# Optimization experiments

Measured on AMD Instinct MI355X. Metric: run time of the kernel, lower is better.

Reference implementation:

```python
import jax, jax.numpy as jnp
import numpy as np

B, C, W, H, D = 1, 2, 192, 192, 192


def setup_inputs() -> dict:
    key = jax.random.key(0)
    k1, k2 = jax.random.split(key)
    x = jax.random.normal(k1, (B, C, W, H, D), dtype=jnp.float32)
    # voxel coordinates, slightly outside the FOV to exercise dct2 boundary
    sizes = jnp.array([W, H, D], dtype=jnp.float32)
    u = jax.random.uniform(k2, (B, W, H, D, 3), dtype=jnp.float32)
    grid = u * (sizes + 3.0) - 2.0  # range [-2, n+1]
    return {"x": x, "grid": grid}


def _reflect_dct2(i, n):
    # dct2 / 'reflect' boundary: symmetric about -0.5 and n-0.5, period 2n
    p = 2 * n
    i = jnp.mod(i, p)  # nonnegative result
    return jnp.where(i >= n, p - 1 - i, i)


def reference(x, grid):
    """grid_pull with linear interpolation, dct2 bound, extrapolate=True.
    x: (B, C, W, H, D); grid: (B, W, H, D, 3) in voxel coords -> (B, C, W, H, D)."""
    Bx, Cx, Wx, Hx, Dx = x.shape
    lo = jnp.floor(grid).astype(jnp.int32)          # (B, W, H, D, 3)
    frac = grid - lo.astype(grid.dtype)             # (B, W, H, D, 3)
    flat = x.reshape(Bx, Cx, Wx * Hx * Dx)
    N = grid.shape[1] * grid.shape[2] * grid.shape[3]
    out = jnp.zeros((Bx, Cx, N), dtype=x.dtype)
    for dx in (0, 1):
        wx = frac[..., 0] if dx else 1.0 - frac[..., 0]
        ix = _reflect_dct2(lo[..., 0] + dx, Wx)
        for dy in (0, 1):
            wy = frac[..., 1] if dy else 1.0 - frac[..., 1]
            iy = _reflect_dct2(lo[..., 1] + dy, Hx)
            for dz in (0, 1):
                wz = frac[..., 2] if dz else 1.0 - frac[..., 2]
                iz = _reflect_dct2(lo[..., 2] + dz, Dx)
                idx = ((ix * Hx + iy) * Dx + iz).reshape(Bx, 1, N)
                vals = jnp.take_along_axis(flat, idx, axis=2)  # (B, C, N)
                w = (wx * wy * wz).reshape(Bx, 1, N)
                out = out + vals * w
    return out.reshape(Bx, Cx, *grid.shape[1:4])
```

## Files before the change

### kernel.cpp

```cpp
#include <hip/hip_runtime.h>
#include <hip/hip_fp16.h>


constexpr int DIM = 192;
constexpr int N = DIM * DIM * DIM;
constexpr int C = 2;

typedef float floatx4 __attribute__((ext_vector_type(4)));

__device__ __forceinline__ int reflect_dct2(int i, int n) {
    const int p = 2 * n;
    i = ((i % p) + p) % p;
    return (i >= n) ? (p - 1 - i) : i;
}

constexpr size_t HALO_BRICKS = (size_t)(DIM / 4) * DIM * DIM;
constexpr size_t HALO_BYTES  = HALO_BRICKS * 64;

constexpr int LDS_STRIDE = 200;

__global__ __launch_bounds__(256) void repack_halo_kernel(
        const float* __restrict__ x,
        uint32_t* __restrict__ xb) {
    __shared__ float lds[16 * LDS_STRIDE];

    const int bxy = blockIdx.x;
    const int y   = bxy % DIM;
    const int bx  = bxy / DIM;
    const int tid = threadIdx.x;

#pragma unroll
    for (int k = 0; k < 3; ++k) {
        const int vidx = tid + k * 256;
        const int r    = vidx / 48;
        const int c4   = vidx - r * 48;
        const int c    = r >> 3;
        const int sx   = (r >> 1) & 3;
        const int ysel = r & 1;
        const int ysrc = min(y + ysel, DIM - 1);
        const size_t src = (size_t)c * N
                         + ((size_t)((bx * 4 + sx) * DIM + ysrc)) * DIM
                         + (size_t)c4 * 4;
        const floatx4 v = __builtin_nontemporal_load((const floatx4*)(x + src));
        *(floatx4*)(&lds[r * LDS_STRIDE + c4 * 4]) = v;
    }
    __syncthreads();

#pragma unroll
    for (int k = 0; k < 3; ++k) {
        const int t  = tid + k * 256;
        const int z  = t >> 2;
        const int q  = t & 3;
        const int zp = min(z + 1, DIM - 1);
        const int r00 = q * 2;
        const int r01 = q * 2 + 1;
        const int r10 = 8 + q * 2;
        const int r11 = 8 + q * 2 + 1;
        uint4 v;
        v.x = __builtin_bit_cast(uint32_t,
              __floats2half2_rn(lds[r00 * LDS_STRIDE + z],  lds[r10 * LDS_STRIDE + z]));
        v.y = __builtin_bit_cast(uint32_t,
              __floats2half2_rn(lds[r00 * LDS_STRIDE + zp], lds[r10 * LDS_STRIDE + zp]));
        v.z = __builtin_bit_cast(uint32_t,
              __floats2half2_rn(lds[r01 * LDS_STRIDE + z],  lds[r11 * LDS_STRIDE + z]));
        v.w = __builtin_bit_cast(uint32_t,
              __floats2half2_rn(lds[r01 * LDS_STRIDE + zp], lds[r11 * LDS_STRIDE + zp]));
        ((uint4*)xb)[(size_t)bxy * (DIM * 4) + t] = v;
    }
}

__global__ __launch_bounds__(256) void grid_pull_halo_kernel(
        const uint32_t* __restrict__ xb,
        const float* __restrict__ grid,
        float* __restrict__ out) {
    const int n = blockIdx.x * blockDim.x + threadIdx.x;
    if (n >= N) return;

    const float gx = __builtin_nontemporal_load(&grid[3 * n + 0]);
    const float gy = __builtin_nontemporal_load(&grid[3 * n + 1]);
    const float gz = __builtin_nontemporal_load(&grid[3 * n + 2]);

    const float fx = floorf(gx), fy = floorf(gy), fz = floorf(gz);
    const int lx = (int)fx, ly = (int)fy, lz = (int)fz;
    const float tx = gx - fx, ty = gy - fy, tz = gz - fz;

    const int ix0 = reflect_dct2(lx,     DIM);
    const int ix1 = reflect_dct2(lx + 1, DIM);
    const int iy0 = reflect_dct2(ly,     DIM);
    const int iy1 = reflect_dct2(ly + 1, DIM);
    const int iz0 = reflect_dct2(lz,     DIM);
    const int iz1 = reflect_dct2(lz + 1, DIM);

    const int ya = min(iy0, iy1), za = min(iz0, iz1);
    const int sy0 = iy0 - ya, sy1 = iy1 - ya;
    const int sz0 = iz0 - za, sz1 = iz1 - za;

    const float wy0 = 1.0f - ty, wy1 = ty;
    const float wz0 = 1.0f - tz, wz1 = tz;

    const float Y0 = (sy0 ? 0.0f : wy0) + (sy1 ? 0.0f : wy1);
    const float Y1 = (sy0 ? wy0 : 0.0f) + (sy1 ? wy1 : 0.0f);
    const float Z0 = (sz0 ? 0.0f : wz0) + (sz1 ? 0.0f : wz1);
    const float Z1 = (sz0 ? wz0 : 0.0f) + (sz1 ? wz1 : 0.0f);

    const size_t d0 = ((size_t)(((ix0 >> 2) * DIM + ya) * DIM + za) << 4) + ((ix0 & 3) << 2);
    const size_t d1 = ((size_t)(((ix1 >> 2) * DIM + ya) * DIM + za) << 4) + ((ix1 & 3) << 2);
    const uint4 v0 = *(const uint4*)(xb + d0);
    const uint4 v1 = *(const uint4*)(xb + d1);

    const float2 a00 = __half22float2(__builtin_bit_cast(__half2, v0.x));
    const float2 a01 = __half22float2(__builtin_bit_cast(__half2, v0.y));
    const float2 a10 = __half22float2(__builtin_bit_cast(__half2, v0.z));
    const float2 a11 = __half22float2(__builtin_bit_cast(__half2, v0.w));
    const float2 b00 = __half22float2(__builtin_bit_cast(__half2, v1.x));
    const float2 b01 = __half22float2(__builtin_bit_cast(__half2, v1.y));
    const float2 b10 = __half22float2(__builtin_bit_cast(__half2, v1.z));
    const float2 b11 = __half22float2(__builtin_bit_cast(__half2, v1.w));

    const float wx0 = 1.0f - tx, wx1 = tx;

    const float acc0 = wx0 * (Y0 * (Z0 * a00.x + Z1 * a01.x) + Y1 * (Z0 * a10.x + Z1 * a11.x))
                     + wx1 * (Y0 * (Z0 * b00.x + Z1 * b01.x) + Y1 * (Z0 * b10.x + Z1 * b11.x));
    const float acc1 = wx0 * (Y0 * (Z0 * a00.y + Z1 * a01.y) + Y1 * (Z0 * a10.y + Z1 * a11.y))
                     + wx1 * (Y0 * (Z0 * b00.y + Z1 * b01.y) + Y1 * (Z0 * b10.y + Z1 * b11.y));

    __builtin_nontemporal_store(acc0, &out[n]);
    __builtin_nontemporal_store(acc1, &out[N + n]);
}

constexpr int NBX = DIM / 4;
constexpr int NBY = DIM / 2;
constexpr int NBZ = DIM / 2;
constexpr int NBRICKS = NBX * NBY * NBZ;
constexpr int XSTRIDE = NBY * NBZ * 16;
constexpr int YSTRIDE = NBZ * 16;
constexpr int ZSTRIDE = 16;

__device__ __forceinline__ int xterm(int ix) { return (ix >> 2) * XSTRIDE + ((ix & 3) << 2); }
__device__ __forceinline__ int yterm(int iy) { return (iy >> 1) * YSTRIDE + ((iy & 1) << 1); }
__device__ __forceinline__ int zterm(int iz) { return (iz >> 1) * ZSTRIDE + (iz & 1); }

__global__ __launch_bounds__(256) void repack_brick_lds_kernel(
        const float* __restrict__ x,
        uint32_t* __restrict__ xb) {
    __shared__ float lds[16 * LDS_STRIDE];

    const int bxy = blockIdx.x;
    const int by  = bxy % NBY;
    const int bx  = bxy / NBY;
    const int tid = threadIdx.x;

#pragma unroll
    for (int k = 0; k < 3; ++k) {
        const int vidx = tid + k * 256;
        const int r    = vidx / 48;
        const int c4   = vidx - r * 48;
        const int c    = r >> 3;
        const int sx   = (r >> 1) & 3;
        const int sy   = r & 1;
        const size_t src = (size_t)c * N
                         + ((size_t)((bx * 4 + sx) * DIM + (by * 2 + sy))) * DIM
                         + (size_t)c4 * 4;
        const floatx4 v = __builtin_nontemporal_load((const floatx4*)(x + src));
        *(floatx4*)(&lds[r * LDS_STRIDE + c4 * 4]) = v;
    }
    __syncthreads();

    for (int slot = tid; slot < NBZ * 4; slot += 256) {
        const int bz = slot >> 2;
        const int q  = slot & 3;
        const int iz = bz * 2;
        const float2 a00 = *(const float2*)&lds[(((0 << 3) | (q << 1) | 0) * LDS_STRIDE) + iz];
        const float2 a01 = *(const float2*)&lds[(((0 << 3) | (q << 1) | 1) * LDS_STRIDE) + iz];
        const float2 a10 = *(const float2*)&lds[(((1 << 3) | (q << 1) | 0) * LDS_STRIDE) + iz];
        const float2 a11 = *(const float2*)&lds[(((1 << 3) | (q << 1) | 1) * LDS_STRIDE) + iz];
        uint4 v;
        v.x = __builtin_bit_cast(uint32_t, __floats2half2_rn(a00.x, a10.x));
        v.y = __builtin_bit_cast(uint32_t, __floats2half2_rn(a00.y, a10.y));
        v.z = __builtin_bit_cast(uint32_t, __floats2half2_rn(a01.x, a11.x));
        v.w = __builtin_bit_cast(uint32_t, __floats2half2_rn(a01.y, a11.y));
        ((uint4*)xb)[(size_t)bxy * (NBZ * 4) + slot] = v;
    }
}

__global__ __launch_bounds__(256) void grid_pull_brick_kernel(
        const uint32_t* __restrict__ xb,
        const float* __restrict__ grid,
        float* __restrict__ out) {
    const int n = blockIdx.x * blockDim.x + threadIdx.x;
    if (n >= N) return;

    const float gx = __builtin_nontemporal_load(&grid[3 * n + 0]);
    const float gy = __builtin_nontemporal_load(&grid[3 * n + 1]);
    const float gz = __builtin_nontemporal_load(&grid[3 * n + 2]);

    const float fx = floorf(gx), fy = floorf(gy), fz = floorf(gz);
    const int lx = (int)fx, ly = (int)fy, lz = (int)fz;
    const float tx = gx - fx, ty = gy - fy, tz = gz - fz;

    const int ix0 = reflect_dct2(lx,     DIM);
    const int ix1 = reflect_dct2(lx + 1, DIM);
    const int iy0 = reflect_dct2(ly,     DIM);
    const int iy1 = reflect_dct2(ly + 1, DIM);
    const int iz0 = reflect_dct2(lz,     DIM);
    const int iz1 = reflect_dct2(lz + 1, DIM);

    const int tx0 = xterm(ix0), tx1 = xterm(ix1);
    const int ty0 = yterm(iy0), ty1 = yterm(iy1);
    const int tz0 = zterm(iz0), tz1 = zterm(iz1);

    const uint32_t u000 = xb[tx0 + ty0 + tz0];
    const uint32_t u001 = xb[tx0 + ty0 + tz1];
    const uint32_t u010 = xb[tx0 + ty1 + tz0];
    const uint32_t u011 = xb[tx0 + ty1 + tz1];
    const uint32_t u100 = xb[tx1 + ty0 + tz0];
    const uint32_t u101 = xb[tx1 + ty0 + tz1];
    const uint32_t u110 = xb[tx1 + ty1 + tz0];
    const uint32_t u111 = xb[tx1 + ty1 + tz1];

    const float wx0 = 1.0f - tx, wx1 = tx;
    const float wy0 = 1.0f - ty, wy1 = ty;
    const float wz0 = 1.0f - tz, wz1 = tz;

    const float w000 = wx0 * wy0 * wz0, w001 = wx0 * wy0 * wz1;
    const float w010 = wx0 * wy1 * wz0, w011 = wx0 * wy1 * wz1;
    const float w100 = wx1 * wy0 * wz0, w101 = wx1 * wy0 * wz1;
    const float w110 = wx1 * wy1 * wz0, w111 = wx1 * wy1 * wz1;

    const float2 f000 = __half22float2(__builtin_bit_cast(__half2, u000));
    const float2 f001 = __half22float2(__builtin_bit_cast(__half2, u001));
    const float2 f010 = __half22float2(__builtin_bit_cast(__half2, u010));
    const float2 f011 = __half22float2(__builtin_bit_cast(__half2, u011));
    const float2 f100 = __half22float2(__builtin_bit_cast(__half2, u100));
    const float2 f101 = __half22float2(__builtin_bit_cast(__half2, u101));
    const float2 f110 = __half22float2(__builtin_bit_cast(__half2, u110));
    const float2 f111 = __half22float2(__builtin_bit_cast(__half2, u111));

    const float acc0 = f000.x * w000 + f001.x * w001 + f010.x * w010 + f011.x * w011
                     + f100.x * w100 + f101.x * w101 + f110.x * w110 + f111.x * w111;
    const float acc1 = f000.y * w000 + f001.y * w001 + f010.y * w010 + f011.y * w011
                     + f100.y * w100 + f101.y * w101 + f110.y * w110 + f111.y * w111;

    __builtin_nontemporal_store(acc0, &out[n]);
    __builtin_nontemporal_store(acc1, &out[N + n]);
}

__global__ __launch_bounds__(256) void grid_pull_planar_kernel(
        const float* __restrict__ x,
        const float* __restrict__ grid,
        float* __restrict__ out) {
    const int n = blockIdx.x * blockDim.x + threadIdx.x;
    if (n >= N) return;

    const float gx = grid[3 * n + 0];
    const float gy = grid[3 * n + 1];
    const float gz = grid[3 * n + 2];

    const float fx = floorf(gx), fy = floorf(gy), fz = floorf(gz);
    const int lx = (int)fx, ly = (int)fy, lz = (int)fz;
    const float tx = gx - fx, ty = gy - fy, tz = gz - fz;

    const int ix0 = reflect_dct2(lx,     DIM);
    const int ix1 = reflect_dct2(lx + 1, DIM);
    const int iy0 = reflect_dct2(ly,     DIM);
    const int iy1 = reflect_dct2(ly + 1, DIM);
    const int iz0 = reflect_dct2(lz,     DIM);
    const int iz1 = reflect_dct2(lz + 1, DIM);

    const float wx0 = 1.0f - tx, wx1 = tx;
    const float wy0 = 1.0f - ty, wy1 = ty;
    const float wz0 = 1.0f - tz, wz1 = tz;

    const int bx0 = ix0 * (DIM * DIM), bx1 = ix1 * (DIM * DIM);
    const int by0 = iy0 * DIM,         by1 = iy1 * DIM;

    const float w000 = wx0 * wy0 * wz0, w001 = wx0 * wy0 * wz1;
    const float w010 = wx0 * wy1 * wz0, w011 = wx0 * wy1 * wz1;
    const float w100 = wx1 * wy0 * wz0, w101 = wx1 * wy0 * wz1;
    const float w110 = wx1 * wy1 * wz0, w111 = wx1 * wy1 * wz1;

#pragma unroll
    for (int c = 0; c < C; ++c) {
        const float* __restrict__ xc = x + (size_t)c * N;
        float acc = xc[bx0 + by0 + iz0] * w000;
        acc += xc[bx0 + by0 + iz1] * w001;
        acc += xc[bx0 + by1 + iz0] * w010;
        acc += xc[bx0 + by1 + iz1] * w011;
        acc += xc[bx1 + by0 + iz0] * w100;
        acc += xc[bx1 + by0 + iz1] * w101;
        acc += xc[bx1 + by1 + iz0] * w110;
        acc += xc[bx1 + by1 + iz1] * w111;
        out[(size_t)c * N + n] = acc;
    }
}

extern "C" void kernel_launch(void* const* d_in, const int* in_sizes, int n_in,
                              void* d_out, int out_size, void* d_ws, size_t ws_size,
                              hipStream_t stream) {
    const float* x    = (const float*)d_in[0];
    const float* grid = (const float*)d_in[1];
    float* out        = (float*)d_out;

    const int threads = 256;
    const int gblocks = (N + threads - 1) / threads;
    const size_t need_brick = (size_t)NBRICKS * 64;

    if (ws_size >= HALO_BYTES) {
        uint32_t* xb = (uint32_t*)d_ws;
        repack_halo_kernel<<<(DIM / 4) * DIM, threads, 0, stream>>>(x, xb);
        grid_pull_halo_kernel<<<gblocks, threads, 0, stream>>>(xb, grid, out);
    } else if (ws_size >= need_brick) {
        uint32_t* xb = (uint32_t*)d_ws;
        repack_brick_lds_kernel<<<NBX * NBY, threads, 0, stream>>>(x, xb);
        grid_pull_brick_kernel<<<gblocks, threads, 0, stream>>>(xb, grid, out);
    } else {
        grid_pull_planar_kernel<<<gblocks, threads, 0, stream>>>(x, grid, out);
    }
}
```

Baseline: 338.2 us.

## Process two y rows per repack block and four voxels per pull thread

The halo repack kernel now handles two consecutive y rows per block, loading three source rows per x/channel into shared memory instead of two per single row. This cuts redundant global reads of the shared y+1 row. The pull kernel gives each thread four consecutive voxels, using three 16-byte vector loads of the grid and vector nontemporal stores of the outputs. This raises memory-level parallelism but increases register use and may lower occupancy.

```diff
diff --git a/kernel.cpp b/kernel.cpp
--- a/kernel.cpp
+++ b/kernel.cpp
@@ -19,43 +19,50 @@
 
 constexpr int LDS_STRIDE = 200;
 
-__global__ __launch_bounds__(256) void repack_halo_kernel(
+__global__ __launch_bounds__(256) void repack_halo2_kernel(
         const float* __restrict__ x,
         uint32_t* __restrict__ xb) {
-    __shared__ float lds[16 * LDS_STRIDE];
-
-    const int bxy = blockIdx.x;
-    const int y   = bxy % DIM;
-    const int bx  = bxy / DIM;
+    __shared__ float lds[24 * LDS_STRIDE];
+
+    const int blk = blockIdx.x;
+    const int yp  = blk % (DIM / 2);
+    const int bx  = blk / (DIM / 2);
+    const int y0  = yp * 2;
     const int tid = threadIdx.x;
 
 #pragma unroll
-    for (int k = 0; k < 3; ++k) {
+    for (int k = 0; k < 5; ++k) {
         const int vidx = tid + k * 256;
-        const int r    = vidx / 48;
-        const int c4   = vidx - r * 48;
-        const int c    = r >> 3;
-        const int sx   = (r >> 1) & 3;
-        const int ysel = r & 1;
-        const int ysrc = min(y + ysel, DIM - 1);
-        const size_t src = (size_t)c * N
-                         + ((size_t)((bx * 4 + sx) * DIM + ysrc)) * DIM
-                         + (size_t)c4 * 4;
-        const floatx4 v = __builtin_nontemporal_load((const floatx4*)(x + src));
-        *(floatx4*)(&lds[r * LDS_STRIDE + c4 * 4]) = v;
+        if (vidx < 24 * 48) {
+            const int r    = vidx / 48;
+            const int c4   = vidx - r * 48;
+            const int c    = r / 12;
+            const int rem  = r - c * 12;
+            const int sx   = rem / 3;
+            const int rsel = rem - sx * 3;
+            const int ysrc = min(y0 + rsel, DIM - 1);
+            const size_t src = (size_t)c * N
+                             + ((size_t)((bx * 4 + sx) * DIM + ysrc)) * DIM
+                             + (size_t)c4 * 4;
+            const floatx4 v = __builtin_nontemporal_load((const floatx4*)(x + src));
+            *(floatx4*)(&lds[r * LDS_STRIDE + c4 * 4]) = v;
+        }
     }
     __syncthreads();
 
 #pragma unroll
-    for (int k = 0; k < 3; ++k) {
+    for (int k = 0; k < 6; ++k) {
         const int t  = tid + k * 256;
-        const int z  = t >> 2;
+        const int a  = t >> 10;
         const int q  = t & 3;
+        const int az = t >> 2;
+        const int aa = az / DIM;
+        const int z  = az - aa * DIM;
         const int zp = min(z + 1, DIM - 1);
-        const int r00 = q * 2;
-        const int r01 = q * 2 + 1;
-        const int r10 = 8 + q * 2;
-        const int r11 = 8 + q * 2 + 1;
+        const int r00 = q * 3 + aa;
+        const int r01 = q * 3 + aa + 1;
+        const int r10 = 12 + q * 3 + aa;
+        const int r11 = 12 + q * 3 + aa + 1;
         uint4 v;
         v.x = __builtin_bit_cast(uint32_t,
               __floats2half2_rn(lds[r00 * LDS_STRIDE + z],  lds[r10 * LDS_STRIDE + z]));
@@ -65,67 +72,83 @@
               __floats2half2_rn(lds[r01 * LDS_STRIDE + z],  lds[r11 * LDS_STRIDE + z]));
         v.w = __builtin_bit_cast(uint32_t,
               __floats2half2_rn(lds[r01 * LDS_STRIDE + zp], lds[r11 * LDS_STRIDE + zp]));
-        ((uint4*)xb)[(size_t)bxy * (DIM * 4) + t] = v;
-    }
-}
-
-__global__ __launch_bounds__(256) void grid_pull_halo_kernel(
+        const size_t brick = ((size_t)(bx * DIM + (y0 + aa)) * DIM + z);
+        ((uint4*)xb)[brick * 4 + q] = v;
+    }
+}
+
+__global__ __launch_bounds__(256) void grid_pull_halo4_kernel(
         const uint32_t* __restrict__ xb,
         const float* __restrict__ grid,
         float* __restrict__ out) {
-    const int n = blockIdx.x * blockDim.x + threadIdx.x;
-    if (n >= N) return;
-
-    const float gx = __builtin_nontemporal_load(&grid[3 * n + 0]);
-    const float gy = __builtin_nontemporal_load(&grid[3 * n + 1]);
-    const float gz = __builtin_nontemporal_load(&grid[3 * n + 2]);
-
-    const float fx = floorf(gx), fy = floorf(gy), fz = floorf(gz);
-    const int lx = (int)fx, ly = (int)fy, lz = (int)fz;
-    const float tx = gx - fx, ty = gy - fy, tz = gz - fz;
-
-    const int ix0 = reflect_dct2(lx,     DIM);
-    const int ix1 = reflect_dct2(lx + 1, DIM);
-    const int iy0 = reflect_dct2(ly,     DIM);
-    const int iy1 = reflect_dct2(ly + 1, DIM);
-    const int iz0 = reflect_dct2(lz,     DIM);
-    const int iz1 = reflect_dct2(lz + 1, DIM);
-
-    const int ya = min(iy0, iy1), za = min(iz0, iz1);
-    const int sy0 = iy0 - ya, sy1 = iy1 - ya;
-    const int sz0 = iz0 - za, sz1 = iz1 - za;
-
-    const float wy0 = 1.0f - ty, wy1 = ty;
-    const float wz0 = 1.0f - tz, wz1 = tz;
-
-    const float Y0 = (sy0 ? 0.0f : wy0) + (sy1 ? 0.0f : wy1);
-    const float Y1 = (sy0 ? wy0 : 0.0f) + (sy1 ? wy1 : 0.0f);
-    const float Z0 = (sz0 ? 0.0f : wz0) + (sz1 ? 0.0f : wz1);
-    const float Z1 = (sz0 ? wz0 : 0.0f) + (sz1 ? wz1 : 0.0f);
-
-    const size_t d0 = ((size_t)(((ix0 >> 2) * DIM + ya) * DIM + za) << 4) + ((ix0 & 3) << 2);
-    const size_t d1 = ((size_t)(((ix1 >> 2) * DIM + ya) * DIM + za) << 4) + ((ix1 & 3) << 2);
-    const uint4 v0 = *(const uint4*)(xb + d0);
-    const uint4 v1 = *(const uint4*)(xb + d1);
-
-    const float2 a00 = __half22float2(__builtin_bit_cast(__half2, v0.x));
-    const float2 a01 = __half22float2(__builtin_bit_cast(__half2, v0.y));
-    const float2 a10 = __half22float2(__builtin_bit_cast(__half2, v0.z));
-    const float2 a11 = __half22float2(__builtin_bit_cast(__half2, v0.w));
-    const float2 b00 = __half22float2(__builtin_bit_cast(__half2, v1.x));
-    const float2 b01 = __half22float2(__builtin_bit_cast(__half2, v1.y));
-    const float2 b10 = __half22float2(__builtin_bit_cast(__half2, v1.z));
-    const float2 b11 = __half22float2(__builtin_bit_cast(__half2, v1.w));
-
-    const float wx0 = 1.0f - tx, wx1 = tx;
-
-    const float acc0 = wx0 * (Y0 * (Z0 * a00.x + Z1 * a01.x) + Y1 * (Z0 * a10.x + Z1 * a11.x))
-                     + wx1 * (Y0 * (Z0 * b00.x + Z1 * b01.x) + Y1 * (Z0 * b10.x + Z1 * b11.x));
-    const float acc1 = wx0 * (Y0 * (Z0 * a00.y + Z1 * a01.y) + Y1 * (Z0 * a10.y + Z1 * a11.y))
-                     + wx1 * (Y0 * (Z0 * b00.y + Z1 * b01.y) + Y1 * (Z0 * b10.y + Z1 * b11.y));
-
-    __builtin_nontemporal_store(acc0, &out[n]);
-    __builtin_nontemporal_store(acc1, &out[N + n]);
+    const int tg = blockIdx.x * blockDim.x + threadIdx.x;
+    if (tg >= N / 4) return;
+
+    const floatx4* gp = (const floatx4*)(grid + (size_t)tg * 12);
+    const floatx4 ga = __builtin_nontemporal_load(gp + 0);
+    const floatx4 gb = __builtin_nontemporal_load(gp + 1);
+    const floatx4 gc = __builtin_nontemporal_load(gp + 2);
+
+    const float gx[4] = {ga.x, ga.w, gb.z, gc.y};
+    const float gy[4] = {ga.y, gb.x, gb.w, gc.z};
+    const float gz[4] = {ga.z, gb.y, gc.x, gc.w};
+
+    uint4 v0[4], v1[4];
+    float WX0[4], WX1[4], Y0[4], Y1[4], Z0[4], Z1[4];
+
+#pragma unroll
+    for (int s = 0; s < 4; ++s) {
+        const float fx = floorf(gx[s]), fy = floorf(gy[s]), fz = floorf(gz[s]);
+        const int lx = (int)fx, ly = (int)fy, lz = (int)fz;
+        const float tx = gx[s] - fx, ty = gy[s] - fy, tz = gz[s] - fz;
+
+        const int ix0 = reflect_dct2(lx,     DIM);
+        const int ix1 = reflect_dct2(lx + 1, DIM);
+        const int iy0 = reflect_dct2(ly,     DIM);
+        const int iy1 = reflect_dct2(ly + 1, DIM);
+        const int iz0 = reflect_dct2(lz,     DIM);
+        const int iz1 = reflect_dct2(lz + 1, DIM);
+
+        const int ya = min(iy0, iy1), za = min(iz0, iz1);
+        const int sy0 = iy0 - ya, sy1 = iy1 - ya;
+        const int sz0 = iz0 - za, sz1 = iz1 - za;
+
+        const float wy0 = 1.0f - ty, wy1 = ty;
+        const float wz0 = 1.0f - tz, wz1 = tz;
+
+        Y0[s] = (sy0 ? 0.0f : wy0) + (sy1 ? 0.0f : wy1);
+        Y1[s] = (sy0 ? wy0 : 0.0f) + (sy1 ? wy1 : 0.0f);
+        Z0[s] = (sz0 ? 0.0f : wz0) + (sz1 ? 0.0f : wz1);
+        Z1[s] = (sz0 ? wz0 : 0.0f) + (sz1 ? wz1 : 0.0f);
+        WX0[s] = 1.0f - tx;
+        WX1[s] = tx;
+
+        const size_t d0 = ((size_t)(((ix0 >> 2) * DIM + ya) * DIM + za) << 4) + ((ix0 & 3) << 2);
+        const size_t d1 = ((size_t)(((ix1 >> 2) * DIM + ya) * DIM + za) << 4) + ((ix1 & 3) << 2);
+        v0[s] = *(const uint4*)(xb + d0);
+        v1[s] = *(const uint4*)(xb + d1);
+    }
+
+    floatx4 acc0, acc1;
+#pragma unroll
+    for (int s = 0; s < 4; ++s) {
+        const float2 a00 = __half22float2(__builtin_bit_cast(__half2, v0[s].x));
+        const float2 a01 = __half22float2(__builtin_bit_cast(__half2, v0[s].y));
+        const float2 a10 = __half22float2(__builtin_bit_cast(__half2, v0[s].z));
+        const float2 a11 = __half22float2(__builtin_bit_cast(__half2, v0[s].w));
+        const float2 b00 = __half22float2(__builtin_bit_cast(__half2, v1[s].x));
+        const float2 b01 = __half22float2(__builtin_bit_cast(__half2, v1[s].y));
+        const float2 b10 = __half22float2(__builtin_bit_cast(__half2, v1[s].z));
+        const float2 b11 = __half22float2(__builtin_bit_cast(__half2, v1[s].w));
+
+        acc0[s] = WX0[s] * (Y0[s] * (Z0[s] * a00.x + Z1[s] * a01.x) + Y1[s] * (Z0[s] * a10.x + Z1[s] * a11.x))
+                + WX1[s] * (Y0[s] * (Z0[s] * b00.x + Z1[s] * b01.x) + Y1[s] * (Z0[s] * b10.x + Z1[s] * b11.x));
+        acc1[s] = WX0[s] * (Y0[s] * (Z0[s] * a00.y + Z1[s] * a01.y) + Y1[s] * (Z0[s] * a10.y + Z1[s] * a11.y))
+                + WX1[s] * (Y0[s] * (Z0[s] * b00.y + Z1[s] * b01.y) + Y1[s] * (Z0[s] * b10.y + Z1[s] * b11.y));
+    }
+
+    __builtin_nontemporal_store(acc0, (floatx4*)(out + (size_t)tg * 4));
+    __builtin_nontemporal_store(acc1, (floatx4*)(out + (size_t)N + (size_t)tg * 4));
 }
 
 constexpr int NBX = DIM / 4;
@@ -302,18 +325,20 @@
     float* out        = (float*)d_out;
 
     const int threads = 256;
-    const int gblocks = (N + threads - 1) / threads;
     const size_t need_brick = (size_t)NBRICKS * 64;
 
     if (ws_size >= HALO_BYTES) {
         uint32_t* xb = (uint32_t*)d_ws;
-        repack_halo_kernel<<<(DIM / 4) * DIM, threads, 0, stream>>>(x, xb);
-        grid_pull_halo_kernel<<<gblocks, threads, 0, stream>>>(xb, grid, out);
+        repack_halo2_kernel<<<(DIM / 4) * (DIM / 2), threads, 0, stream>>>(x, xb);
+        const int gblocks = (N / 4 + threads - 1) / threads;
+        grid_pull_halo4_kernel<<<gblocks, threads, 0, stream>>>(xb, grid, out);
     } else if (ws_size >= need_brick) {
         uint32_t* xb = (uint32_t*)d_ws;
         repack_brick_lds_kernel<<<NBX * NBY, threads, 0, stream>>>(x, xb);
+        const int gblocks = (N + threads - 1) / threads;
         grid_pull_brick_kernel<<<gblocks, threads, 0, stream>>>(xb, grid, out);
     } else {
+        const int gblocks = (N + threads - 1) / threads;
         grid_pull_planar_kernel<<<gblocks, threads, 0, stream>>>(x, grid, out);
     }
 }
```

After: 350.0 us. 1.03x slower.
